# Optimization experiments

Hardware: AMD Instinct MI355X
Metric: run time of the kernel (lower is better)

## Reference

```python
import jax, jax.numpy as jnp
import numpy as np

N_NODES = 50000
N_EDGES = 500000
NFEAT = 128
NHID = 128
NOUT = 16


def setup_inputs() -> dict:
    key = jax.random.key(0)
    ks = jax.random.split(key, 8)
    x = jax.random.normal(ks[0], (N_NODES, NFEAT), dtype=jnp.float32)
    edge_src = jax.random.randint(ks[1], (N_EDGES,), 0, N_NODES, dtype=jnp.int32)
    edge_dst = jax.random.randint(ks[2], (N_EDGES,), 0, N_NODES, dtype=jnp.int32)
    edge_weight = jax.random.uniform(ks[3], (N_EDGES,), dtype=jnp.float32)
    # Glorot-ish init for linear weights, zero bias (PyG GCNConv default bias=0)
    def glorot(k, fan_in, fan_out):
        s = jnp.sqrt(6.0 / (fan_in + fan_out))
        return jax.random.uniform(k, (fan_in, fan_out), jnp.float32, -s, s)
    W1 = glorot(ks[4], NFEAT, NHID)
    W2 = glorot(ks[5], NHID, NHID)
    W3 = glorot(ks[6], NHID, NOUT)
    b1 = jnp.zeros((NHID,), jnp.float32)
    b2 = jnp.zeros((NHID,), jnp.float32)
    b3 = jnp.zeros((NOUT,), jnp.float32)
    return {"x": x, "edge_src": edge_src, "edge_dst": edge_dst,
            "edge_weight": edge_weight, "W1": W1, "b1": b1,
            "W2": W2, "b2": b2, "W3": W3, "b3": b3}


def gcn_conv(x, src, dst, ew, W, b):
    """PyG GCNConv: symmetric-normalized aggregation with self-loops (weight 1).

    out_i = sum_{(j->i)} d_i^{-1/2} w_ji d_j^{-1/2} (x_j W) + d_i^{-1} (x_i W) + b
    where d_i = 1 + sum of incoming edge weights.
    """
    n = x.shape[0]
    xw = x @ W                                            # [N, F_out]
    deg = jax.ops.segment_sum(ew, dst, num_segments=n) + 1.0  # self-loop weight 1
    dinv = jnp.where(deg > 0, jax.lax.rsqrt(deg), 0.0)    # d^{-1/2}
    norm = dinv[src] * ew * dinv[dst]                     # [E]
    agg = jax.ops.segment_sum(xw[src] * norm[:, None], dst, num_segments=n)
    self_loop = xw * (dinv * dinv)[:, None]               # d_i^{-1} * x_i W
    return agg + self_loop + b


def reference(x, edge_src, edge_dst, edge_weight, W1, b1, W2, b2, W3, b3):
    # Dropout layers are identity in eval mode.
    h = gcn_conv(x, edge_src, edge_dst, edge_weight, W1, b1)
    h = jax.nn.relu(h)
    h = gcn_conv(h, edge_src, edge_dst, edge_weight, W2, b2)
    h = jax.nn.relu(h)
    h = gcn_conv(h, edge_src, edge_dst, edge_weight, W3, b3)
    return jax.nn.log_softmax(h, axis=1)
```

## Files before the change

kernel.cpp:

```cpp
#include <hip/hip_runtime.h>
#include <math.h>

#define NN 50000
#define NE 500000
#define NF 128
#define NO 16
#define SCAN_B 1024
#define NB_SCAN 49
#define NPART 16
#define EBL 1954

static_assert(NN < 65536, "src must fit u16");

typedef _Float16 f16x8 __attribute__((ext_vector_type(8)));
typedef _Float16 f16x4 __attribute__((ext_vector_type(4)));
typedef float f32x4 __attribute__((ext_vector_type(4)));

union HU { unsigned short u; _Float16 h; };

__device__ inline float rec_w(unsigned int rec) {
    HU cu; cu.u = (unsigned short)(rec >> 16);
    return (float)cu.h;
}


__global__ void k_count_rank(const int* __restrict__ dst, const float* __restrict__ ew,
                             int* __restrict__ pcnt, float* __restrict__ pdeg,
                             int* __restrict__ rank, int E,
                             const float* __restrict__ W1, const float* __restrict__ W2,
                             _Float16* __restrict__ W1T, _Float16* __restrict__ W2T) {
    int b = blockIdx.x;
    if (b < EBL) {
        int part = b & (NPART - 1);
        int e = b * 256 + threadIdx.x;
        if (e < E) {
            int d = dst[e];
            rank[e] = atomicAdd(&pcnt[part * NN + d], 1);
            atomicAdd(&pdeg[part * NN + d], ew[e]);
        }
    } else {
        int idx = (b - EBL) * 256 + threadIdx.x;
        int r = idx >> 7, c = idx & 127;
        W1T[(size_t)c * NF + r] = (_Float16)W1[idx];
        W2T[(size_t)c * NF + r] = (_Float16)W2[idx];
    }
}

__global__ void k_scan1f(int* __restrict__ pcnt, const float* __restrict__ pdeg,
                         int* __restrict__ offs_p, int* __restrict__ bsums,
                         float* __restrict__ dinv, int* __restrict__ done) {
    __shared__ int sm[SCAN_B];
    __shared__ int isLast;
    int t = threadIdx.x;
    int i = blockIdx.x * SCAN_B + t;
    int c = 0;
    if (i < NN) {
        int run = 0;
#pragma unroll
        for (int p = 0; p < NPART; ++p) {
            int v = pcnt[p * NN + i];
            pcnt[p * NN + i] = run;
            run += v;
        }
        c = run;
        float deg = 1.0f;
#pragma unroll
        for (int p = 0; p < NPART; ++p) deg += pdeg[p * NN + i];
        dinv[i] = rsqrtf(deg);
    }
    sm[t] = c;
    __syncthreads();
    for (int off = 1; off < SCAN_B; off <<= 1) {
        int x = (t >= off) ? sm[t - off] : 0;
        __syncthreads();
        sm[t] += x;
        __syncthreads();
    }
    if (i < NN) offs_p[i] = sm[t] - c;
    if (t == SCAN_B - 1) {
        __hip_atomic_store(&bsums[blockIdx.x], sm[t], __ATOMIC_RELEASE,
                           __HIP_MEMORY_SCOPE_AGENT);
        int old = __hip_atomic_fetch_add(done, 1, __ATOMIC_ACQ_REL,
                                         __HIP_MEMORY_SCOPE_AGENT);
        isLast = (old == (int)gridDim.x - 1) ? 1 : 0;
    }
    __syncthreads();
    if (isLast && t < 64) {
        int v = (t < NB_SCAN) ? __hip_atomic_load(&bsums[t], __ATOMIC_ACQUIRE,
                                                  __HIP_MEMORY_SCOPE_AGENT) : 0;
        int orig = v;
#pragma unroll
        for (int off = 1; off < 64; off <<= 1) {
            int u = __shfl_up(v, off, 64);
            if (t >= off) v += u;
        }
        if (t < NB_SCAN)
            __hip_atomic_store(&bsums[t], v - orig, __ATOMIC_RELEASE,
                               __HIP_MEMORY_SCOPE_AGENT);
    }
}

__global__ void k_scatter(const int* __restrict__ src, const int* __restrict__ dst,
                          const float* __restrict__ ew, const int* __restrict__ pcnt,
                          const int* __restrict__ rank,
                          const int* __restrict__ offs_p, const int* __restrict__ bsums,
                          unsigned int* __restrict__ erec, int E) {
    int part = blockIdx.x & (NPART - 1);
    int e = blockIdx.x * blockDim.x + threadIdx.x;
    if (e < E) {
        int d = dst[e];
        int pos = offs_p[d] + bsums[d >> 10] + pcnt[part * NN + d] + rank[e];
        HU cu; cu.h = (_Float16)ew[e];
        erec[pos] = (unsigned int)src[e] | ((unsigned int)cu.u << 16);
    }
}


__device__ inline f16x8 afrag_load(const float* X, int row, int k0) {
    const float4* p = (const float4*)(X + (size_t)row * NF + k0);
    float4 a = p[0], b = p[1];
    f16x8 r;
    r[0] = (_Float16)a.x; r[1] = (_Float16)a.y; r[2] = (_Float16)a.z; r[3] = (_Float16)a.w;
    r[4] = (_Float16)b.x; r[5] = (_Float16)b.y; r[6] = (_Float16)b.z; r[7] = (_Float16)b.w;
    return r;
}
__device__ inline f16x8 afrag_load(const _Float16* X, int row, int k0) {
    return *(const f16x8*)(X + (size_t)row * NF + k0);
}

template <typename TA>
__global__ __launch_bounds__(256) void k_gemm_mfma(const TA* __restrict__ X,
                                                   const _Float16* __restrict__ WT,
                                                   const float* __restrict__ dinv,
                                                   _Float16* __restrict__ Z, int M) {
    __shared__ _Float16 ls[4][16 * 136];
    const int tid  = threadIdx.x;
    const int w    = tid >> 6;
    const int lane = tid & 63;
    const int n16  = lane & 15;
    const int quad = lane >> 4;
    const int r0   = blockIdx.x * 64 + w * 16;

    int arow = r0 + n16; if (arow > M - 1) arow = M - 1;

    f32x4 acc[8];
#pragma unroll
    for (int c = 0; c < 8; ++c) acc[c] = (f32x4){0.f, 0.f, 0.f, 0.f};

#pragma unroll
    for (int kk = 0; kk < 4; ++kk) {
        int k0 = kk * 32 + quad * 8;
        f16x8 a = afrag_load(X, arow, k0);
#pragma unroll
        for (int c = 0; c < 8; ++c) {
            f16x8 b = *(const f16x8*)(WT + (size_t)(c * 16 + n16) * NF + k0);
            acc[c] = __builtin_amdgcn_mfma_f32_16x16x32_f16(a, b, acc[c], 0, 0, 0);
        }
    }

#pragma unroll
    for (int reg = 0; reg < 4; ++reg) {
        int lrow = quad * 4 + reg;
        int grow = r0 + lrow; if (grow > M - 1) grow = M - 1;
        float di = dinv[grow];
#pragma unroll
        for (int c = 0; c < 8; ++c)
            ls[w][lrow * 136 + c * 16 + n16] = (_Float16)(acc[c][reg] * di);
    }
    __syncthreads();
#pragma unroll
    for (int i = 0; i < 4; ++i) {
        int off16 = i * 64 + lane;
        int row = off16 >> 4;
        int col = off16 & 15;
        int grow = r0 + row;
        if (grow < M) {
            f16x8 v = *(const f16x8*)(&ls[w][row * 136 + col * 8]);
            *(f16x8*)(Z + (size_t)grow * NF + col * 8) = v;
        }
    }
}

__global__ __launch_bounds__(256) void k_agg128h(const _Float16* __restrict__ z,
                                                 const float* __restrict__ dinv,
                                                 const int* __restrict__ offs_p,
                                                 const int* __restrict__ bsums,
                                                 const unsigned int* __restrict__ erec,
                                                 const float* __restrict__ bias,
                                                 _Float16* __restrict__ hout, int relu) {
    const int tid  = threadIdx.x;
    const int lane = tid & 63;
    const int half = lane >> 5;
    const int li   = lane & 31;
    int n = __builtin_amdgcn_readfirstlane(blockIdx.x * 4 + (tid >> 6));

    float acc0 = 0.f, acc1 = 0.f, acc2 = 0.f, acc3 = 0.f;

    int s = offs_p[n] + bsums[n >> 10];
    int e = (n + 1 < NN) ? offs_p[n + 1] + bsums[(n + 1) >> 10] : NE;
    for (int base = s; base < e; base += 64) {
        int cnt = e - base; if (cnt > 64) cnt = 64;
        unsigned int rec = 0u;
        if (lane < cnt) rec = __builtin_nontemporal_load(erec + base + lane);
        int   my_s = rec & 0xFFFF;
        float my_w = rec_w(rec);
        int k = 0;
        for (; k + 7 < cnt; k += 8) {
            int e0 = k + half, e1 = k + 2 + half, e2 = k + 4 + half, e3 = k + 6 + half;
            int s0 = __shfl(my_s, e0, 64), s1 = __shfl(my_s, e1, 64);
            int s2 = __shfl(my_s, e2, 64), s3 = __shfl(my_s, e3, 64);
            float w0 = __shfl(my_w, e0, 64), w1 = __shfl(my_w, e1, 64);
            float w2 = __shfl(my_w, e2, 64), w3 = __shfl(my_w, e3, 64);
            f16x4 v0 = *(const f16x4*)(z + ((size_t)s0 << 7) + li * 4);
            f16x4 v1 = *(const f16x4*)(z + ((size_t)s1 << 7) + li * 4);
            f16x4 v2 = *(const f16x4*)(z + ((size_t)s2 << 7) + li * 4);
            f16x4 v3 = *(const f16x4*)(z + ((size_t)s3 << 7) + li * 4);
            acc0 = fmaf((float)v0[0], w0, acc0); acc1 = fmaf((float)v0[1], w0, acc1);
            acc2 = fmaf((float)v0[2], w0, acc2); acc3 = fmaf((float)v0[3], w0, acc3);
            acc0 = fmaf((float)v1[0], w1, acc0); acc1 = fmaf((float)v1[1], w1, acc1);
            acc2 = fmaf((float)v1[2], w1, acc2); acc3 = fmaf((float)v1[3], w1, acc3);
            acc0 = fmaf((float)v2[0], w2, acc0); acc1 = fmaf((float)v2[1], w2, acc1);
            acc2 = fmaf((float)v2[2], w2, acc2); acc3 = fmaf((float)v2[3], w2, acc3);
            acc0 = fmaf((float)v3[0], w3, acc0); acc1 = fmaf((float)v3[1], w3, acc1);
            acc2 = fmaf((float)v3[2], w3, acc2); acc3 = fmaf((float)v3[3], w3, acc3);
        }
        for (; k < cnt; k += 2) {
            int eidx = k + half;
            int ec = eidx < cnt ? eidx : cnt - 1;
            int   s0 = __shfl(my_s, ec, 64);
            float wt = __shfl(my_w, ec, 64);
            float w0 = (eidx < cnt) ? wt : 0.0f;
            f16x4 v0 = *(const f16x4*)(z + ((size_t)s0 << 7) + li * 4);
            acc0 = fmaf((float)v0[0], w0, acc0); acc1 = fmaf((float)v0[1], w0, acc1);
            acc2 = fmaf((float)v0[2], w0, acc2); acc3 = fmaf((float)v0[3], w0, acc3);
        }
    }
    acc0 += __shfl_xor(acc0, 32, 64);
    acc1 += __shfl_xor(acc1, 32, 64);
    acc2 += __shfl_xor(acc2, 32, 64);
    acc3 += __shfl_xor(acc3, 32, 64);

    f16x4 sv = *(const f16x4*)(z + ((size_t)n << 7) + li * 4);
    float di = dinv[n];
    float4 bb = *(const float4*)(bias + li * 4);
    float r0 = fmaf(di, (float)sv[0] + acc0, bb.x);
    float r1 = fmaf(di, (float)sv[1] + acc1, bb.y);
    float r2 = fmaf(di, (float)sv[2] + acc2, bb.z);
    float r3 = fmaf(di, (float)sv[3] + acc3, bb.w);
    if (relu) {
        r0 = fmaxf(r0, 0.0f); r1 = fmaxf(r1, 0.0f);
        r2 = fmaxf(r2, 0.0f); r3 = fmaxf(r3, 0.0f);
    }
    if (half == 0) {
        f16x4 o;
        o[0] = (_Float16)r0; o[1] = (_Float16)r1;
        o[2] = (_Float16)r2; o[3] = (_Float16)r3;
        __builtin_nontemporal_store(o, (f16x4*)(hout + ((size_t)n << 7) + li * 4));
    }
}

__global__ __launch_bounds__(256) void k_gemm16(const _Float16* __restrict__ H,
                                                const float* __restrict__ W3,
                                                const float* __restrict__ dinv,
                                                _Float16* __restrict__ Z3, int M) {
    __shared__ float Wl[NF * NO];
    __shared__ float Hs[16 * 132];
    int tid = threadIdx.x;
    for (int i = tid; i < NF * NO; i += 256) Wl[i] = W3[i];
    int n0 = blockIdx.x * 16;
    {
        int row = tid >> 4, h8 = tid & 15;
        int gr = n0 + row; if (gr > M - 1) gr = M - 1;
        f16x8 v = *(const f16x8*)(H + (size_t)gr * NF + h8 * 8);
        float4 f0 = {(float)v[0], (float)v[1], (float)v[2], (float)v[3]};
        float4 f1 = {(float)v[4], (float)v[5], (float)v[6], (float)v[7]};
        *(float4*)(&Hs[row * 132 + h8 * 8])     = f0;
        *(float4*)(&Hs[row * 132 + h8 * 8 + 4]) = f1;
    }
    __syncthreads();
    int ln = tid >> 4, c = tid & 15;
    float acc = 0.0f;
#pragma unroll 8
    for (int k = 0; k < NF; ++k) acc = fmaf(Hs[ln * 132 + k], Wl[k * NO + c], acc);
    int n = n0 + ln;
    if (n < M) Z3[(size_t)n * NO + c] = (_Float16)(acc * dinv[n]);
}

__global__ __launch_bounds__(256) void k_agg16_ls(const _Float16* __restrict__ z3,
                                                  const float* __restrict__ dinv,
                                                  const int* __restrict__ offs_p,
                                                  const int* __restrict__ bsums,
                                                  const unsigned int* __restrict__ erec,
                                                  const float* __restrict__ bias,
                                                  float* __restrict__ out) {
    int tid = threadIdx.x;
    int ln = tid >> 4, c = tid & 15;
    int n = blockIdx.x * 16 + ln;
    float acc = (float)z3[((size_t)n << 4) + c];
    int s = offs_p[n] + bsums[n >> 10];
    int e = (n + 1 < NN) ? offs_p[n + 1] + bsums[(n + 1) >> 10] : NE;
    int j = s;
    for (; j + 1 < e; j += 2) {
        unsigned int r0 = erec[j], r1 = erec[j + 1];
        acc = fmaf((float)z3[((size_t)(r0 & 0xFFFF) << 4) + c], rec_w(r0), acc);
        acc = fmaf((float)z3[((size_t)(r1 & 0xFFFF) << 4) + c], rec_w(r1), acc);
    }
    if (j < e) {
        unsigned int r0 = erec[j];
        acc = fmaf((float)z3[((size_t)(r0 & 0xFFFF) << 4) + c], rec_w(r0), acc);
    }
    acc = fmaf(dinv[n], acc, bias[c]);
    float m = acc;
#pragma unroll
    for (int off = 8; off > 0; off >>= 1) m = fmaxf(m, __shfl_xor(m, off, 16));
    float ex = expf(acc - m);
    float ss = ex;
#pragma unroll
    for (int off = 8; off > 0; off >>= 1) ss += __shfl_xor(ss, off, 16);
    out[(size_t)n * NO + c] = acc - m - logf(ss);
}


extern "C" void kernel_launch(void* const* d_in, const int* in_sizes, int n_in,
                              void* d_out, int out_size, void* d_ws, size_t ws_size,
                              hipStream_t stream) {
    const float* x   = (const float*)d_in[0];
    const int*   esrc= (const int*)  d_in[1];
    const int*   edst= (const int*)  d_in[2];
    const float* ew  = (const float*)d_in[3];
    const float* W1  = (const float*)d_in[4];
    const float* b1  = (const float*)d_in[5];
    const float* W2  = (const float*)d_in[6];
    const float* b2  = (const float*)d_in[7];
    const float* W3  = (const float*)d_in[8];
    const float* b3  = (const float*)d_in[9];
    float* out = (float*)d_out;

    char* p = (char*)d_ws;
    _Float16* z   = (_Float16*)p; p += (size_t)NN * NF * 2;
    _Float16* h   = (_Float16*)p; p += (size_t)NN * NF * 2;
    _Float16* z3  = (_Float16*)p; p += (size_t)NN * NO * 2;
    float* dinv   = (float*)p; p += (size_t)NN * 4;
    unsigned int* erec = (unsigned int*)p; p += (size_t)NE * 4;
    int*   rank   = (int*)p;   p += (size_t)NE * 4;
    int*   pcnt   = (int*)p;   p += (size_t)NPART * NN * 4;
    float* pdeg   = (float*)p; p += (size_t)NPART * NN * 4;
    int*   done   = (int*)p;   p += 64;
    int*   offs_p = (int*)p;   p += (size_t)(NN + 1) * 4;
    int*   bsums  = (int*)p;   p += 256;
    _Float16* W1T = (_Float16*)p; p += (size_t)NF * NF * 2;
    _Float16* W2T = (_Float16*)p; p += (size_t)NF * NF * 2;

    hipMemsetAsync(pcnt, 0, (size_t)NPART * NN * 4 * 2 + 64, stream);

    k_count_rank<<<EBL + 64, 256, 0, stream>>>(edst, ew, pcnt, pdeg, rank, NE,
                                               W1, W2, W1T, W2T);
    k_scan1f<<<NB_SCAN, SCAN_B, 0, stream>>>(pcnt, pdeg, offs_p, bsums, dinv, done);
    k_scatter<<<EBL, 256, 0, stream>>>(esrc, edst, ew, pcnt, rank, offs_p, bsums, erec, NE);

    k_gemm_mfma<float><<<(NN + 63) / 64, 256, 0, stream>>>(x, W1T, dinv, z, NN);
    k_agg128h<<<NN / 4, 256, 0, stream>>>(z, dinv, offs_p, bsums, erec, b1, h, 1);
    k_gemm_mfma<_Float16><<<(NN + 63) / 64, 256, 0, stream>>>(h, W2T, dinv, z, NN);
    k_agg128h<<<NN / 4, 256, 0, stream>>>(z, dinv, offs_p, bsums, erec, b2, h, 1);
    k_gemm16<<<(NN + 15) / 16, 256, 0, stream>>>(h, W3, dinv, z3, NN);
    k_agg16_ls<<<NN / 16, 256, 0, stream>>>(z3, dinv, offs_p, bsums, erec, b3, out);
}
```

Before: 273.3 us.

## Drop float-atomic degree accumulation; compute dinv from CSR after scatter

```diff
diff --git a/kernel.cpp b/kernel.cpp
--- a/kernel.cpp
+++ b/kernel.cpp
@@ -8,7 +8,8 @@
 #define SCAN_B 1024
 #define NB_SCAN 49
 #define NPART 16
-#define EBL 1954
+#define EB4 489
+#define EB2 977
 
 static_assert(NN < 65536, "src must fit u16");
 
@@ -24,31 +25,46 @@
 }
 
 
-__global__ void k_count_rank(const int* __restrict__ dst, const float* __restrict__ ew,
-                             int* __restrict__ pcnt, float* __restrict__ pdeg,
-                             int* __restrict__ rank, int E,
-                             const float* __restrict__ W1, const float* __restrict__ W2,
-                             _Float16* __restrict__ W1T, _Float16* __restrict__ W2T) {
+__global__ __launch_bounds__(256) void k_count_rank(const int* __restrict__ dst,
+                                                    int* __restrict__ pcnt,
+                                                    int* __restrict__ rank, int E,
+                                                    const float* __restrict__ W1,
+                                                    const float* __restrict__ W2,
+                                                    _Float16* __restrict__ W1T,
+                                                    _Float16* __restrict__ W2T) {
     int b = blockIdx.x;
-    if (b < EBL) {
+    if (b < EB4 - 1) {
         int part = b & (NPART - 1);
-        int e = b * 256 + threadIdx.x;
-        if (e < E) {
-            int d = dst[e];
-            rank[e] = atomicAdd(&pcnt[part * NN + d], 1);
-            atomicAdd(&pdeg[part * NN + d], ew[e]);
+        int e0 = b * 1024 + threadIdx.x;
+        int d0 = dst[e0], d1 = dst[e0 + 256], d2 = dst[e0 + 512], d3 = dst[e0 + 768];
+        int r0 = atomicAdd(&pcnt[part * NN + d0], 1);
+        int r1 = atomicAdd(&pcnt[part * NN + d1], 1);
+        int r2 = atomicAdd(&pcnt[part * NN + d2], 1);
+        int r3 = atomicAdd(&pcnt[part * NN + d3], 1);
+        rank[e0]       = r0;
+        rank[e0 + 256] = r1;
+        rank[e0 + 512] = r2;
+        rank[e0 + 768] = r3;
+    } else if (b == EB4 - 1) {
+        int part = b & (NPART - 1);
+#pragma unroll
+        for (int k = 0; k < 4; ++k) {
+            int e = b * 1024 + k * 256 + threadIdx.x;
+            if (e < E) {
+                int d = dst[e];
+                rank[e] = atomicAdd(&pcnt[part * NN + d], 1);
+            }
         }
     } else {
-        int idx = (b - EBL) * 256 + threadIdx.x;
+        int idx = (b - EB4) * 256 + threadIdx.x;
         int r = idx >> 7, c = idx & 127;
         W1T[(size_t)c * NF + r] = (_Float16)W1[idx];
         W2T[(size_t)c * NF + r] = (_Float16)W2[idx];
     }
 }
 
-__global__ void k_scan1f(int* __restrict__ pcnt, const float* __restrict__ pdeg,
-                         int* __restrict__ offs_p, int* __restrict__ bsums,
-                         float* __restrict__ dinv, int* __restrict__ done) {
+__global__ void k_scan1f(int* __restrict__ pcnt, int* __restrict__ offs_p,
+                         int* __restrict__ bsums, int* __restrict__ done) {
     __shared__ int sm[SCAN_B];
     __shared__ int isLast;
     int t = threadIdx.x;
@@ -63,10 +79,6 @@
             run += v;
         }
         c = run;
-        float deg = 1.0f;
-#pragma unroll
-        for (int p = 0; p < NPART; ++p) deg += pdeg[p * NN + i];
-        dinv[i] = rsqrtf(deg);
     }
     sm[t] = c;
     __syncthreads();
@@ -100,18 +112,38 @@
     }
 }
 
-__global__ void k_scatter(const int* __restrict__ src, const int* __restrict__ dst,
-                          const float* __restrict__ ew, const int* __restrict__ pcnt,
-                          const int* __restrict__ rank,
-                          const int* __restrict__ offs_p, const int* __restrict__ bsums,
-                          unsigned int* __restrict__ erec, int E) {
-    int part = blockIdx.x & (NPART - 1);
-    int e = blockIdx.x * blockDim.x + threadIdx.x;
-    if (e < E) {
-        int d = dst[e];
-        int pos = offs_p[d] + bsums[d >> 10] + pcnt[part * NN + d] + rank[e];
-        HU cu; cu.h = (_Float16)ew[e];
-        erec[pos] = (unsigned int)src[e] | ((unsigned int)cu.u << 16);
+__global__ __launch_bounds__(256) void k_scatter(const int* __restrict__ src,
+                                                 const int* __restrict__ dst,
+                                                 const float* __restrict__ ew,
+                                                 const int* __restrict__ pcnt,
+                                                 const int* __restrict__ rank,
+                                                 const int* __restrict__ offs_p,
+                                                 const int* __restrict__ bsums,
+                                                 unsigned int* __restrict__ erec, int E) {
+    int b = blockIdx.x;
+#pragma unroll
+    for (int k = 0; k < 2; ++k) {
+        int e = b * 512 + k * 256 + threadIdx.x;
+        if (e < E) {
+            int part = (e >> 10) & (NPART - 1);
+            int d = dst[e];
+            int pos = offs_p[d] + bsums[d >> 10] + pcnt[part * NN + d] + rank[e];
+            HU cu; cu.h = (_Float16)ew[e];
+            erec[pos] = (unsigned int)src[e] | ((unsigned int)cu.u << 16);
+        }
+    }
+}
+
+__global__ void k_dinv_csr(const unsigned int* __restrict__ erec,
+                           const int* __restrict__ offs_p, const int* __restrict__ bsums,
+                           float* __restrict__ dinv) {
+    int n = blockIdx.x * blockDim.x + threadIdx.x;
+    if (n < NN) {
+        int s = offs_p[n] + bsums[n >> 10];
+        int e = (n + 1 < NN) ? offs_p[n + 1] + bsums[(n + 1) >> 10] : NE;
+        float deg = 1.0f;
+        for (int j = s; j < e; ++j) deg += rec_w(erec[j]);
+        dinv[n] = rsqrtf(deg);
     }
 }
 
@@ -344,19 +376,18 @@
     unsigned int* erec = (unsigned int*)p; p += (size_t)NE * 4;
     int*   rank   = (int*)p;   p += (size_t)NE * 4;
     int*   pcnt   = (int*)p;   p += (size_t)NPART * NN * 4;
-    float* pdeg   = (float*)p; p += (size_t)NPART * NN * 4;
     int*   done   = (int*)p;   p += 64;
     int*   offs_p = (int*)p;   p += (size_t)(NN + 1) * 4;
     int*   bsums  = (int*)p;   p += 256;
     _Float16* W1T = (_Float16*)p; p += (size_t)NF * NF * 2;
     _Float16* W2T = (_Float16*)p; p += (size_t)NF * NF * 2;
 
-    hipMemsetAsync(pcnt, 0, (size_t)NPART * NN * 4 * 2 + 64, stream);
-
-    k_count_rank<<<EBL + 64, 256, 0, stream>>>(edst, ew, pcnt, pdeg, rank, NE,
-                                               W1, W2, W1T, W2T);
-    k_scan1f<<<NB_SCAN, SCAN_B, 0, stream>>>(pcnt, pdeg, offs_p, bsums, dinv, done);
-    k_scatter<<<EBL, 256, 0, stream>>>(esrc, edst, ew, pcnt, rank, offs_p, bsums, erec, NE);
+    hipMemsetAsync(pcnt, 0, (size_t)NPART * NN * 4 + 64, stream);
+
+    k_count_rank<<<EB4 + 64, 256, 0, stream>>>(edst, pcnt, rank, NE, W1, W2, W1T, W2T);
+    k_scan1f<<<NB_SCAN, SCAN_B, 0, stream>>>(pcnt, offs_p, bsums, done);
+    k_scatter<<<EB2, 256, 0, stream>>>(esrc, edst, ew, pcnt, rank, offs_p, bsums, erec, NE);
+    k_dinv_csr<<<(NN + 255) / 256, 256, 0, stream>>>(erec, offs_p, bsums, dinv);
 
     k_gemm_mfma<float><<<(NN + 63) / 64, 256, 0, stream>>>(x, W1T, dinv, z, NN);
     k_agg128h<<<NN / 4, 256, 0, stream>>>(z, dinv, offs_p, bsums, erec, b1, h, 1);
```

Measured after the change: 249.7 us. -8.6%, faster.
